# Kernel tuning notes

Measured on AMD Instinct MI355X. Metric: run time of the kernel, lower is better.

## Reference

```python
import jax, jax.numpy as jnp
import numpy as np

B, T, D, H, Z = 256, 256, 512, 1024, 128
EPS = 1e-6


def _init_params(key):
    ks = jax.random.split(key, 30)
    def w(i, fi, fo):
        return 0.02 * jax.random.normal(ks[i], (fi, fo), dtype=jnp.float32)
    def b(i, fo):
        return 0.01 * jax.random.normal(ks[i], (fo,), dtype=jnp.float32)
    return {
        'phix_w': w(0, D, H), 'phix_b': b(1, H),
        'pm_w1': w(2, H, H), 'pm_b1': b(3, H), 'pm_w2': w(4, H, Z), 'pm_b2': b(5, Z),
        'ps_w1': w(6, H, H), 'ps_b1': b(7, H), 'ps_w2': w(8, H, Z), 'ps_b2': b(9, Z),
        'em_w1': w(10, 2 * H, H), 'em_b1': b(11, H), 'em_w2': w(12, H, Z), 'em_b2': b(13, Z),
        'es_w1': w(14, 2 * H, H), 'es_b1': b(15, H), 'es_w2': w(16, H, Z), 'es_b2': b(17, Z),
        'dm_w1': w(18, H + Z, H), 'dm_b1': b(19, H), 'dm_w2': w(20, H, D), 'dm_b2': b(21, D),
        'gru_wih': w(22, H + Z, 3 * H), 'gru_bih': b(23, 3 * H), 'gru_bhh': b(24, 3 * H),
    }


def setup_inputs() -> dict:
    key = jax.random.key(0)
    kx, ke, kh, kp = jax.random.split(key, 4)
    inp = {
        'x': jax.random.uniform(kx, (B, T, D), dtype=jnp.float32),   # bernoulli-like data in [0,1]
        'eps': jax.random.normal(ke, (T, B, Z), dtype=jnp.float32),  # reparam noise per step
        'h0': jax.random.normal(kh, (B, H), dtype=jnp.float32),      # Variable(th.randn) initial hidden
    }
    inp.update(_init_params(kp))
    return inp


def reference(x, eps, h0, phix_w, phix_b, pm_w1, pm_b1, pm_w2, pm_b2,
              ps_w1, ps_b1, ps_w2, ps_b2, em_w1, em_b1, em_w2, em_b2,
              es_w1, es_b1, es_w2, es_b2, dm_w1, dm_b1, dm_w2, dm_b2,
              gru_wih, gru_bih, gru_bhh):
    relu, sig, sp = jax.nn.relu, jax.nn.sigmoid, jax.nn.softplus

    def step(h, inp):
        x_t, e_t = inp                                            # [B,D], [B,Z]
        phi = relu(x_t @ phix_w + phix_b)                         # phi_x(x_t): [B,H]
        pm = relu(relu(h @ pm_w1 + pm_b1) @ pm_w2 + pm_b2)        # prior mu [B,Z]
        ps = sp(relu(h @ ps_w1 + ps_b1) @ ps_w2 + ps_b2)          # prior std [B,Z]
        hx = jnp.concatenate([h, phi], axis=-1)                   # [B,2H]
        zm = relu(relu(hx @ em_w1 + em_b1) @ em_w2 + em_b2)       # encoder mu
        zs = sp(relu(hx @ es_w1 + es_b1) @ es_w2 + es_b2)         # encoder std
        z = zm + zs * e_t                                         # reparam sample
        hz = jnp.concatenate([h, z], axis=-1)                     # [B,H+Z]
        xm = sig(relu(hz @ dm_w1 + dm_b1) @ dm_w2 + dm_b2)        # decoder mu [B,D]
        # GRU step; source calls self.rnn(...) without a hidden state -> h_prev = 0,
        # so the W_hh@h term vanishes and only b_hh contributes.
        gi = jnp.concatenate([phi, z], axis=-1) @ gru_wih + gru_bih
        gi_r, gi_u, gi_n = jnp.split(gi, 3, axis=-1)
        bh_r, bh_u, bh_n = jnp.split(gru_bhh, 3)
        r = sig(gi_r + bh_r)
        u = sig(gi_u + bh_u)
        n = jnp.tanh(gi_n + r * bh_n)
        h_new = (1.0 - u) * n                                     # (1-u)*n + u*0
        # ELBO: KL(q||p) for diagonal Gaussians + Bernoulli NLL, mean over batch
        kld = jnp.sum(jnp.log(ps + EPS) - jnp.log(zs + EPS)
                      + (zs ** 2 + (zm - pm) ** 2) / (2.0 * ps ** 2 + EPS) - 0.5,
                      axis=-1).mean()
        xm_c = jnp.clip(xm, 1e-6, 1.0 - 1e-6)
        nll = -jnp.sum(x_t * jnp.log(xm_c) + (1.0 - x_t) * jnp.log1p(-xm_c), axis=-1).mean()
        return h_new, (z, zm, zs, xm, kld + nll, kld, nll)

    xs = jnp.swapaxes(x, 0, 1)                                    # [T,B,D]
    _, (Zs, enc_mu, enc_std, dec_mu, loss_t, kld_t, nll_t) = jax.lax.scan(step, h0, (xs, eps))
    loss = loss_t.sum()
    return loss, kld_t[-1], nll_t[-1], Zs, enc_mu, enc_std, dec_mu
```

## Files before the change

kernel.cpp:

```cpp
#include <hip/hip_runtime.h>

typedef unsigned short u16;
typedef __bf16 bf16x8 __attribute__((ext_vector_type(8)));
typedef float f32x4 __attribute__((ext_vector_type(4)));
typedef unsigned uint32x4 __attribute__((ext_vector_type(4)));

#define EPSC 1e-6f

__device__ __forceinline__ float b2f(u16 x) { return __uint_as_float(((unsigned)x) << 16); }
__device__ __forceinline__ u16 f2b(float f) {
    unsigned u = __float_as_uint(f);
    unsigned r = (u + 0x7fffu + ((u >> 16) & 1u)) >> 16;
    return (u16)r;
}
__device__ __forceinline__ float softplusf(float x) {
    return fmaxf(x, 0.f) + log1pf(__expf(-fabsf(x)));
}

__global__ void conv_x4(u16* __restrict__ dst, const float* __restrict__ x) {
    size_t i4 = (size_t)blockIdx.x * 256 + threadIdx.x;
    size_t o = i4 * 4;
    int d = (int)(o & 511);
    int b = (int)((o >> 9) & 255);
    int t = (int)(o >> 17);
    float4 v = *(const float4*)(x + ((size_t)b * 256 + t) * 512 + d);
    unsigned p0 = (unsigned)f2b(v.x) | ((unsigned)f2b(v.y) << 16);
    unsigned p1 = (unsigned)f2b(v.z) | ((unsigned)f2b(v.w) << 16);
    *(uint2*)(dst + o) = make_uint2(p0, p1);
}

__global__ void conv_f32_bf16(u16* __restrict__ dst, const float* __restrict__ src, int n) {
    int i = blockIdx.x * 256 + threadIdx.x;
    if (i < n) dst[i] = f2b(src[i]);
}

__global__ void tr_conv(u16* __restrict__ dst, const float* __restrict__ src,
                        int R, int C, int ld) {
    int idx = blockIdx.x * 256 + threadIdx.x;
    if (idx >= R * C) return;
    int c = idx / R, r = idx % R;
    dst[idx] = f2b(src[(size_t)r * ld + c]);
}

__global__ void conv_fragB(u16* __restrict__ dst, const float* __restrict__ em1,
                           const float* __restrict__ es1) {
    int idx = blockIdx.x * 256 + threadIdx.x;
    int col = idx >> 8, kb = idx & 255;
    int k = kb * 8, ct = col >> 4, lr = col & 15, kq = kb >> 2, lk = kb & 3;
    size_t off = ((size_t)ct * 64 + kq) * 512 + lk * 128 + lr * 8;
    const float* src = (col < 1024) ? em1 : es1;
    const int c = (col < 1024) ? col : col - 1024;
#pragma unroll
    for (int j = 0; j < 8; j++)
        dst[off + j] = f2b(src[(size_t)(k + j) * 1024 + c]);
}

__global__ void conv_fragB2(u16* __restrict__ dst, const float* __restrict__ src) {
    int idx = blockIdx.x * 256 + threadIdx.x;
    int col = idx >> 7, kb = idx & 127;
    int k = kb * 8, ct = col >> 4, lr = col & 15, kq = kb >> 2, lk = kb & 3;
    size_t off = ((size_t)ct * 32 + kq) * 512 + lk * 128 + lr * 8;
#pragma unroll
    for (int j = 0; j < 8; j++)
        dst[off + j] = f2b(src[(size_t)(k + j) * 128 + col]);
}

__global__ void conv_fragG(u16* __restrict__ dst, const float* __restrict__ gwih) {
    int idx = blockIdx.x * 256 + threadIdx.x;
    int gate = idx >> 14, rem = idx & 16383;
    int col = rem >> 4, kb = rem & 15;
    int k = kb * 8, ct = col >> 4, lr = col & 15, kq = kb >> 2, lk = kb & 3;
    size_t off = (size_t)gate * 131072 + ((size_t)ct * 4 + kq) * 512 + lk * 128 + lr * 8;
#pragma unroll
    for (int j = 0; j < 8; j++)
        dst[off + j] = f2b(gwih[(size_t)(1024 + k + j) * 3072 + gate * 1024 + col]);
}

enum { EPI_PARTIAL = 0, EPI_BF16_RELU = 1, EPI_BF16_NONE = 2,
       EPI_F32_RELU = 3, EPI_F32_SP = 4, EPI_F32_SIG = 5, EPI_TGIP = 6 };

template <int EPI>
__global__ __launch_bounds__(256)
void gemm128(const u16* __restrict__ A0, const u16* __restrict__ A1,
             int lda0, int lda1, int kSplit,
             const u16* __restrict__ Wt, int ldw,
             const float* __restrict__ bias,
             u16* __restrict__ Cb, float* __restrict__ Cf,
             int M, int N, int K, int kChunk) {
    __shared__ __align__(16) u16 As[128 * 72];
    __shared__ __align__(16) u16 Bs[128 * 72];
    const int tid = threadIdx.x;
    const int wid = tid >> 6, lane = tid & 63;
    const int wm = wid >> 1, wn = wid & 1;
    const int lr = lane & 15, lk = lane >> 4;
    const int m0 = blockIdx.y * 128, n0 = blockIdx.x * 128;
    const int kBeg = blockIdx.z * kChunk;
    const int rsub = lane >> 3;
    const int csub = (lane & 7) * 8;

    f32x4 acc[4][4];
#pragma unroll
    for (int i = 0; i < 4; i++)
#pragma unroll
        for (int j = 0; j < 4; j++) { f32x4 z = {0.f, 0.f, 0.f, 0.f}; acc[i][j] = z; }

    for (int kt = 0; kt < kChunk; kt += 64) {
        const int k0 = kBeg + kt;
        const u16* Ap; int kk, lda;
        if (k0 < kSplit) { Ap = A0; kk = k0; lda = lda0; }
        else             { Ap = A1; kk = k0 - kSplit; lda = lda1; }
        uint4 ra[4], rb[4];
#pragma unroll
        for (int i = 0; i < 4; i++) {
            const int q = wid * 4 + i;
            const int r = q * 8 + rsub;
            ra[i] = *(const uint4*)(Ap + (size_t)(m0 + r) * lda + kk + csub);
            rb[i] = *(const uint4*)(Wt + (size_t)(n0 + r) * ldw + k0 + csub);
        }
        __syncthreads();
#pragma unroll
        for (int i = 0; i < 4; i++) {
            const int q = wid * 4 + i;
            const int r = q * 8 + rsub;
            *(uint4*)&As[r * 72 + csub] = ra[i];
            *(uint4*)&Bs[r * 72 + csub] = rb[i];
        }
        __syncthreads();
#pragma unroll
        for (int s = 0; s < 2; s++) {
            bf16x8 af[4], bfr[4];
#pragma unroll
            for (int i = 0; i < 4; i++)
                af[i] = *(const bf16x8*)&As[(wm * 64 + i * 16 + lr) * 72 + s * 32 + lk * 8];
#pragma unroll
            for (int j = 0; j < 4; j++)
                bfr[j] = *(const bf16x8*)&Bs[(wn * 64 + j * 16 + lr) * 72 + s * 32 + lk * 8];
#pragma unroll
            for (int i = 0; i < 4; i++)
#pragma unroll
                for (int j = 0; j < 4; j++)
                    acc[i][j] = __builtin_amdgcn_mfma_f32_16x16x32_bf16(af[i], bfr[j], acc[i][j], 0, 0, 0);
        }
    }

    const int rowb = m0 + wm * 64, colb = n0 + wn * 64;
#pragma unroll
    for (int i = 0; i < 4; i++) {
#pragma unroll
        for (int j = 0; j < 4; j++) {
            const int col = colb + j * 16 + lr;
            if (EPI == EPI_TGIP) {
                const int row0 = rowb + i * 16 + lk * 4;
                const int tt = row0 >> 8, b0 = row0 & 255;
                const int gate = col >> 10, cc = col & 1023;
                unsigned lo = (unsigned)f2b(acc[i][j][0]) | ((unsigned)f2b(acc[i][j][1]) << 16);
                unsigned hi = (unsigned)f2b(acc[i][j][2]) | ((unsigned)f2b(acc[i][j][3]) << 16);
                *(uint2*)(Cb + (((size_t)tt * 3 + gate) * 1024 + cc) * 256 + b0) = make_uint2(lo, hi);
            } else {
#pragma unroll
                for (int r = 0; r < 4; r++) {
                    const int row = rowb + i * 16 + lk * 4 + r;
                    float v = acc[i][j][r];
                    if (EPI == EPI_PARTIAL) {
                        Cf[(size_t)blockIdx.z * ((size_t)M * N) + (size_t)row * N + col] = v;
                    } else {
                        if (bias) v += bias[col];
                        if (EPI == EPI_BF16_RELU || EPI == EPI_F32_RELU) v = fmaxf(v, 0.f);
                        else if (EPI == EPI_F32_SP)  v = softplusf(v);
                        else if (EPI == EPI_F32_SIG) v = 1.f / (1.f + __expf(-v));
                        if (EPI == EPI_BF16_RELU || EPI == EPI_BF16_NONE) Cb[(size_t)row * N + col] = f2b(v);
                        else Cf[(size_t)row * N + col] = v;
                    }
                }
            }
        }
    }
}

static constexpr size_t oPHIXWT  = 0;
static constexpr size_t oWCATT   = 1048576;
static constexpr size_t oEMW2T   = 9437184;
static constexpr size_t oESW2T   = 9699328;
static constexpr size_t oWIHPHIT = 9961472;
static constexpr size_t oWIHZT   = 16252928;
static constexpr size_t oPMW1T   = 17039360;
static constexpr size_t oPMW2T   = 19136512;
static constexpr size_t oPSW1T   = 19398656;
static constexpr size_t oPSW2T   = 21495808;
static constexpr size_t oDMW1T   = 21757952;
static constexpr size_t oDMW2T   = 24117248;
static constexpr size_t oHS      = 25165824;
static constexpr size_t oZBF     = 159907840;
static constexpr size_t oT12     = 176685056;
static constexpr size_t oBAR     = 177733632;
static constexpr size_t oKLDT    = 177737728;
static constexpr size_t oNLLT    = 177738752;
static constexpr size_t oPHI     = 177739776;
static constexpr size_t oGIP     = 311957504;
static constexpr size_t WS_NEED  = 714610688;

static constexpr size_t NZ = (size_t)256 * 256 * 128;
static constexpr size_t O_Z  = 3;
static constexpr size_t O_MU = 3 + NZ;
static constexpr size_t O_STD = 3 + 2 * NZ;
static constexpr size_t O_XM = 3 + 3 * NZ;

__global__ __launch_bounds__(256, 1)
void vrnn_step(int t, int prolog,
               const float* __restrict__ eps,
               const float* __restrict__ em_b1, const float* __restrict__ es_b1,
               const float* __restrict__ em_b2, const float* __restrict__ es_b2,
               const float* __restrict__ gbih, const float* __restrict__ gbhh,
               char* ws, float* out) {
    __shared__ __align__(16) u16 POOL[16 * 2056];
    __shared__ float zmL[2048], zsL[2048];
    __shared__ __align__(16) u16 zTH[16 * 136];

    const int bx = blockIdx.x, tid = threadIdx.x;
    const int wid = tid >> 6, lane = tid & 63;
    const int lr = lane & 15, lk = lane >> 4;
    const int g = bx >> 4, n = bx & 15;
    const int r0 = g * 16;

    const u16* wcatF = (const u16*)(ws + oWCATT);
    const u16* em2F  = (const u16*)(ws + oEMW2T);
    const u16* es2F  = (const u16*)(ws + oESW2T);
    const u16* wihZF = (const u16*)(ws + oWIHZT);
    const u16* PHI   = (const u16*)(ws + oPHI);
    const u16* GIPT  = (const u16*)(ws + oGIP);
    u16* HS    = (u16*)(ws + oHS);
    u16* ZBFg  = (u16*)(ws + oZBF);
    u16* T12p0 = (u16*)(ws + oT12);
    u16* T12p1 = (u16*)(ws + oPHIXWT);

    float* outZ  = out + O_Z;
    float* outMu = out + O_MU;
    float* outSd = out + O_STD;

    u16* S12 = POOL;
    u16* hL  = POOL;
    u16* PH  = POOL + 16 * 1032;

    const int srow = tid >> 4, sc8 = (tid & 15) * 8;

    if (!prolog) {
        {
            const u16* src = ((t & 1) ? T12p1 : T12p0) + (size_t)(r0 + srow) * 2048 + sc8;
#pragma unroll
            for (int p = 0; p < 16; p++)
                *(uint32x4*)&S12[srow * 2056 + sc8 + p * 128] = *(const uint32x4*)(src + p * 128);
        }
        __syncthreads();

        {
            const int halfz = wid >> 1, cq = wid & 1;
            const u16* WF = (halfz ? es2F : em2F) + (size_t)(cq * 4) * 16384 + lk * 128 + lr * 8;
            const u16* Sr = &S12[lr * 2056 + halfz * 1024];
            f32x4 az0 = {0.f,0.f,0.f,0.f}, az1 = az0, az2 = az0, az3 = az0;
#pragma unroll 1
            for (int kq = 0; kq < 32; kq++) {
                bf16x8 af = *(const bf16x8*)(Sr + kq * 32 + lk * 8);
                az0 = __builtin_amdgcn_mfma_f32_16x16x32_bf16(af, *(const bf16x8*)(WF + (size_t)kq * 512), az0, 0, 0, 0);
                az1 = __builtin_amdgcn_mfma_f32_16x16x32_bf16(af, *(const bf16x8*)(WF + 16384 + (size_t)kq * 512), az1, 0, 0, 0);
                az2 = __builtin_amdgcn_mfma_f32_16x16x32_bf16(af, *(const bf16x8*)(WF + 32768 + (size_t)kq * 512), az2, 0, 0, 0);
                az3 = __builtin_amdgcn_mfma_f32_16x16x32_bf16(af, *(const bf16x8*)(WF + 49152 + (size_t)kq * 512), az3, 0, 0, 0);
            }
#pragma unroll
            for (int q = 0; q < 4; q++) {
                const f32x4 az = (q == 0) ? az0 : (q == 1) ? az1 : (q == 2) ? az2 : az3;
                const int c = cq * 64 + q * 16 + lr;
#pragma unroll
                for (int r = 0; r < 4; r++) {
                    const int row = lk * 4 + r;
                    if (!halfz) zmL[row * 128 + c] = fmaxf(az[r] + em_b2[c], 0.f);
                    else        zsL[row * 128 + c] = softplusf(az[r] + es_b2[c]);
                }
            }
        }
        __syncthreads();

        {
            const int row = tid >> 4, col = (tid & 15) * 8;
            const size_t o = (size_t)t * 32768 + (size_t)(r0 + row) * 128 + col;
            const float* ep = eps + o;
            float4 e0 = *(const float4*)ep, e1 = *(const float4*)(ep + 4);
            float zmv[8], zsv[8], zv[8];
#pragma unroll
            for (int i = 0; i < 8; i++) {
                zmv[i] = zmL[row * 128 + col + i];
                zsv[i] = zsL[row * 128 + col + i];
                const float ev = (i < 4) ? (&e0.x)[i] : (&e1.x)[i - 4];
                zv[i] = zmv[i] + zsv[i] * ev;
            }
            uint32x4 zp;
#pragma unroll
            for (int j = 0; j < 4; j++)
                zp[j] = (unsigned)f2b(zv[2 * j]) | ((unsigned)f2b(zv[2 * j + 1]) << 16);
            *(uint32x4*)&zTH[row * 136 + col] = zp;
            if (n == 0) {
#pragma unroll
                for (int i = 0; i < 8; i++) {
                    outMu[o + i] = zmv[i];
                    outSd[o + i] = zsv[i];
                    outZ[o + i]  = zv[i];
                }
                *(uint32x4*)(ZBFg + o) = zp;
            }
        }
        __syncthreads();

        {
            bf16x8 zf0 = *(const bf16x8*)&zTH[lr * 136 + lk * 8];
            bf16x8 zf1 = *(const bf16x8*)&zTH[lr * 136 + 32 + lk * 8];
            bf16x8 zf2 = *(const bf16x8*)&zTH[lr * 136 + 64 + lk * 8];
            bf16x8 zf3 = *(const bf16x8*)&zTH[lr * 136 + 96 + lk * 8];
            const u16* gT = GIPT + (size_t)t * 786432;
#pragma unroll 1
            for (int i = 0; i < 16; i++) {
                const int ct = wid * 16 + i;
                const int col = ct * 16 + lr;
                const u16* bR = wihZF + (size_t)ct * 2048 + lk * 128 + lr * 8;
                const u16* bU = bR + 131072;
                const u16* bN = bU + 131072;
                f32x4 aR = {0.f,0.f,0.f,0.f}, aU = aR, aN = aR;
                aR = __builtin_amdgcn_mfma_f32_16x16x32_bf16(zf0, *(const bf16x8*)(bR), aR, 0, 0, 0);
                aR = __builtin_amdgcn_mfma_f32_16x16x32_bf16(zf1, *(const bf16x8*)(bR + 512), aR, 0, 0, 0);
                aR = __builtin_amdgcn_mfma_f32_16x16x32_bf16(zf2, *(const bf16x8*)(bR + 1024), aR, 0, 0, 0);
                aR = __builtin_amdgcn_mfma_f32_16x16x32_bf16(zf3, *(const bf16x8*)(bR + 1536), aR, 0, 0, 0);
                aU = __builtin_amdgcn_mfma_f32_16x16x32_bf16(zf0, *(const bf16x8*)(bU), aU, 0, 0, 0);
                aU = __builtin_amdgcn_mfma_f32_16x16x32_bf16(zf1, *(const bf16x8*)(bU + 512), aU, 0, 0, 0);
                aU = __builtin_amdgcn_mfma_f32_16x16x32_bf16(zf2, *(const bf16x8*)(bU + 1024), aU, 0, 0, 0);
                aU = __builtin_amdgcn_mfma_f32_16x16x32_bf16(zf3, *(const bf16x8*)(bU + 1536), aU, 0, 0, 0);
                aN = __builtin_amdgcn_mfma_f32_16x16x32_bf16(zf0, *(const bf16x8*)(bN), aN, 0, 0, 0);
                aN = __builtin_amdgcn_mfma_f32_16x16x32_bf16(zf1, *(const bf16x8*)(bN + 512), aN, 0, 0, 0);
                aN = __builtin_amdgcn_mfma_f32_16x16x32_bf16(zf2, *(const bf16x8*)(bN + 1024), aN, 0, 0, 0);
                aN = __builtin_amdgcn_mfma_f32_16x16x32_bf16(zf3, *(const bf16x8*)(bN + 1536), aN, 0, 0, 0);
                const size_t gb = (size_t)col * 256 + r0 + lk * 4;
                uint2 gR2 = *(const uint2*)(gT + gb);
                uint2 gU2 = *(const uint2*)(gT + 262144 + gb);
                uint2 gN2 = *(const uint2*)(gT + 524288 + gb);
                const u16 gRv[4] = {(u16)(gR2.x & 0xffff), (u16)(gR2.x >> 16),
                                    (u16)(gR2.y & 0xffff), (u16)(gR2.y >> 16)};
                const u16 gUv[4] = {(u16)(gU2.x & 0xffff), (u16)(gU2.x >> 16),
                                    (u16)(gU2.y & 0xffff), (u16)(gU2.y >> 16)};
                const u16 gNv[4] = {(u16)(gN2.x & 0xffff), (u16)(gN2.x >> 16),
                                    (u16)(gN2.y & 0xffff), (u16)(gN2.y >> 16)};
                const float bihR = gbih[col],        bhR = gbhh[col];
                const float bihU = gbih[1024 + col], bhU = gbhh[1024 + col];
                const float bihN = gbih[2048 + col], bhN = gbhh[2048 + col];
#pragma unroll
                for (int r = 0; r < 4; r++) {
                    const float gr = aR[r] + b2f(gRv[r]) + bihR + bhR;
                    const float gu = aU[r] + b2f(gUv[r]) + bihU + bhU;
                    float gn       = aN[r] + b2f(gNv[r]) + bihN;
                    const float rr_ = 1.f / (1.f + __expf(-gr));
                    const float uu  = 1.f / (1.f + __expf(-gu));
                    gn += rr_ * bhN;
                    const float e2 = __expf(-2.f * fabsf(gn));
                    float th = (1.f - e2) / (1.f + e2);
                    th = (gn < 0.f) ? -th : th;
                    hL[(lk * 4 + r) * 1032 + col] = f2b((1.f - uu) * th);
                }
            }
        }
        __syncthreads();

        if (n == 0) {
            u16* dstH = HS + (size_t)(t + 1) * 262144 + (size_t)(r0 + srow) * 1024 + sc8;
#pragma unroll
            for (int p = 0; p < 8; p++)
                *(uint32x4*)(dstH + p * 128) = *(const uint32x4*)&hL[srow * 1032 + sc8 + p * 128];
        }
    } else {
        const u16* src = HS + (size_t)(r0 + srow) * 1024 + sc8;
#pragma unroll
        for (int p = 0; p < 8; p++)
            *(uint32x4*)&hL[srow * 1032 + sc8 + p * 128] = *(const uint32x4*)(src + p * 128);
        __syncthreads();
    }

    if (t < 255) {
        {
            const u16* psrc = PHI + (size_t)(t + 1) * 262144 + (size_t)(r0 + srow) * 1024 + sc8;
#pragma unroll
            for (int p = 0; p < 8; p++)
                *(uint32x4*)&PH[srow * 1032 + sc8 + p * 128] = *(const uint32x4*)(psrc + p * 128);
        }
        __syncthreads();

        f32x4 a0 = {0.f,0.f,0.f,0.f}, a1 = {0.f,0.f,0.f,0.f};
        const int ct0 = n * 8 + wid * 2;
        const u16* b0s = wcatF + (size_t)ct0 * 32768 + lk * 128 + lr * 8;
        const u16* b1s = b0s + 32768;
#pragma unroll 1
        for (int kq = 0; kq < 32; kq++) {
            bf16x8 af = *(const bf16x8*)&hL[lr * 1032 + kq * 32 + lk * 8];
            a0 = __builtin_amdgcn_mfma_f32_16x16x32_bf16(af, *(const bf16x8*)(b0s + (size_t)kq * 512), a0, 0, 0, 0);
            a1 = __builtin_amdgcn_mfma_f32_16x16x32_bf16(af, *(const bf16x8*)(b1s + (size_t)kq * 512), a1, 0, 0, 0);
        }
#pragma unroll 1
        for (int kq = 32; kq < 64; kq++) {
            bf16x8 af = *(const bf16x8*)&PH[lr * 1032 + (kq - 32) * 32 + lk * 8];
            a0 = __builtin_amdgcn_mfma_f32_16x16x32_bf16(af, *(const bf16x8*)(b0s + (size_t)kq * 512), a0, 0, 0, 0);
            a1 = __builtin_amdgcn_mfma_f32_16x16x32_bf16(af, *(const bf16x8*)(b1s + (size_t)kq * 512), a1, 0, 0, 0);
        }
        __syncthreads();
#pragma unroll
        for (int i = 0; i < 2; i++) {
            const f32x4 a = i ? a1 : a0;
            const int lct = wid * 2 + i;
            const int colg = n * 128 + lct * 16 + lr;
            const float bb = (colg < 1024) ? em_b1[colg] : es_b1[colg - 1024];
#pragma unroll
            for (int r = 0; r < 4; r++)
                zTH[(lk * 4 + r) * 136 + lct * 16 + lr] = f2b(fmaxf(a[r] + bb, 0.f));
        }
        __syncthreads();
        {
            u16* dst = ((t & 1) ? T12p0 : T12p1) + (size_t)(r0 + srow) * 2048 + n * 128 + sc8;
            *(uint32x4*)dst = *(const uint32x4*)&zTH[srow * 136 + sc8];
        }
    }
}

__global__ __launch_bounds__(256)
void loss_per_t(const float* __restrict__ x,
                const float* __restrict__ xm,
                const float* __restrict__ zm, const float* __restrict__ zs,
                const float* __restrict__ pm, const float* __restrict__ ps,
                float* __restrict__ kldT, float* __restrict__ nllT) {
    const int t = blockIdx.x, bb = threadIdx.x;
    float kld = 0.f, nll = 0.f;
    const size_t ozb = ((size_t)t * 256 + bb) * 128;
    for (int zz = 0; zz < 128; zz++) {
        const float qs = zs[ozb + zz], qm = zm[ozb + zz];
        const float pmv = pm[ozb + zz], psv = ps[ozb + zz];
        const float d = qm - pmv;
        kld += logf(psv + EPSC) - logf(qs + EPSC)
             + (qs * qs + d * d) / (2.f * psv * psv + EPSC) - 0.5f;
    }
    const size_t oxb = ((size_t)t * 256 + bb) * 512;
    const size_t oxi = ((size_t)bb * 256 + t) * 512;
    for (int dd = 0; dd < 512; dd++) {
        const float xv = x[oxi + dd];
        float m = xm[oxb + dd];
        m = fminf(fmaxf(m, 1e-6f), 1.f - 1e-6f);
        nll -= xv * logf(m) + (1.f - xv) * log1pf(-m);
    }
    __shared__ float sk[256], sn[256];
    sk[bb] = kld; sn[bb] = nll;
    __syncthreads();
    for (int s = 128; s > 0; s >>= 1) {
        if (bb < s) { sk[bb] += sk[bb + s]; sn[bb] += sn[bb + s]; }
        __syncthreads();
    }
    if (bb == 0) { kldT[t] = sk[0] / 256.f; nllT[t] = sn[0] / 256.f; }
}

__global__ __launch_bounds__(256)
void loss_final(const float* __restrict__ kldT, const float* __restrict__ nllT,
                float* __restrict__ out) {
    const int tid = threadIdx.x;
    __shared__ float s[256];
    s[tid] = kldT[tid] + nllT[tid];
    __syncthreads();
    for (int st = 128; st > 0; st >>= 1) {
        if (tid < st) s[tid] += s[tid + st];
        __syncthreads();
    }
    if (tid == 0) { out[0] = s[0]; out[1] = kldT[255]; out[2] = nllT[255]; }
}

extern "C" void kernel_launch(void* const* d_in, const int* in_sizes, int n_in,
                              void* d_out, int out_size, void* d_ws, size_t ws_size,
                              hipStream_t stream) {
    const float* x      = (const float*)d_in[0];
    const float* eps    = (const float*)d_in[1];
    const float* h0     = (const float*)d_in[2];
    const float* phix_w = (const float*)d_in[3];
    const float* phix_b = (const float*)d_in[4];
    const float* pm_w1  = (const float*)d_in[5];
    const float* pm_b1  = (const float*)d_in[6];
    const float* pm_w2  = (const float*)d_in[7];
    const float* pm_b2  = (const float*)d_in[8];
    const float* ps_w1  = (const float*)d_in[9];
    const float* ps_b1  = (const float*)d_in[10];
    const float* ps_w2  = (const float*)d_in[11];
    const float* ps_b2  = (const float*)d_in[12];
    const float* em_w1  = (const float*)d_in[13];
    const float* em_b1  = (const float*)d_in[14];
    const float* em_w2  = (const float*)d_in[15];
    const float* em_b2  = (const float*)d_in[16];
    const float* es_w1  = (const float*)d_in[17];
    const float* es_b1  = (const float*)d_in[18];
    const float* es_w2  = (const float*)d_in[19];
    const float* es_b2  = (const float*)d_in[20];
    const float* dm_w1  = (const float*)d_in[21];
    const float* dm_b1  = (const float*)d_in[22];
    const float* dm_w2  = (const float*)d_in[23];
    const float* dm_b2  = (const float*)d_in[24];
    const float* gwih   = (const float*)d_in[25];
    const float* gbih   = (const float*)d_in[26];
    const float* gbhh   = (const float*)d_in[27];
    float* out = (float*)d_out;

    if (ws_size < WS_NEED) return;
    char* w = (char*)d_ws;
    u16* phixWt  = (u16*)(w + oPHIXWT);
    u16* wcatF   = (u16*)(w + oWCATT);
    u16* em2F    = (u16*)(w + oEMW2T);
    u16* es2F    = (u16*)(w + oESW2T);
    u16* wihPhiT = (u16*)(w + oWIHPHIT);
    u16* wihZF   = (u16*)(w + oWIHZT);
    u16* pmW1T   = (u16*)(w + oPMW1T);
    u16* pmW2T   = (u16*)(w + oPMW2T);
    u16* psW1T   = (u16*)(w + oPSW1T);
    u16* psW2T   = (u16*)(w + oPSW2T);
    u16* dmW1T   = (u16*)(w + oDMW1T);
    u16* dmW2T   = (u16*)(w + oDMW2T);
    u16* HS      = (u16*)(w + oHS);
    u16* ZBF     = (u16*)(w + oZBF);
    u16* PHI     = (u16*)(w + oPHI);
    u16* GIPT    = (u16*)(w + oGIP);
    u16* XbfT    = (u16*)(w + oGIP);
    float* PMbuf = (float*)(w + oGIP);
    float* PSbuf = (float*)(w + oGIP + 33554432);
    float* kldT  = (float*)(w + oKLDT);
    float* nllT  = (float*)(w + oNLLT);

    conv_x4<<<32768, 256, 0, stream>>>(XbfT, x);
    conv_f32_bf16<<<1024, 256, 0, stream>>>(HS, h0, 262144);
    tr_conv<<<2048, 256, 0, stream>>>(phixWt, phix_w, 512, 1024, 1024);
    conv_fragB<<<2048, 256, 0, stream>>>(wcatF, em_w1, es_w1);
    conv_fragB2<<<64, 256, 0, stream>>>(em2F, em_w2);
    conv_fragB2<<<64, 256, 0, stream>>>(es2F, es_w2);
    tr_conv<<<12288, 256, 0, stream>>>(wihPhiT, gwih, 1024, 3072, 3072);
    conv_fragG<<<192, 256, 0, stream>>>(wihZF, gwih);
    tr_conv<<<4096, 256, 0, stream>>>(pmW1T, pm_w1, 1024, 1024, 1024);
    tr_conv<<<512, 256, 0, stream>>>(pmW2T, pm_w2, 1024, 128, 128);
    tr_conv<<<4096, 256, 0, stream>>>(psW1T, ps_w1, 1024, 1024, 1024);
    tr_conv<<<512, 256, 0, stream>>>(psW2T, ps_w2, 1024, 128, 128);
    tr_conv<<<4608, 256, 0, stream>>>(dmW1T, dm_w1, 1152, 1024, 1024);
    tr_conv<<<2048, 256, 0, stream>>>(dmW2T, dm_w2, 1024, 512, 512);

    gemm128<EPI_BF16_RELU><<<dim3(8, 512, 1), 256, 0, stream>>>(
        XbfT, nullptr, 512, 0, 512, phixWt, 512, phix_b, PHI, nullptr, 65536, 1024, 512, 512);
    gemm128<EPI_TGIP><<<dim3(24, 512, 1), 256, 0, stream>>>(
        PHI, nullptr, 1024, 0, 1024, wihPhiT, 1024, nullptr, GIPT, nullptr, 65536, 3072, 1024, 1024);

    vrnn_step<<<256, 256, 0, stream>>>(-1, 1, eps, em_b1, es_b1, em_b2, es_b2,
                                       gbih, gbhh, (char*)d_ws, out);
    for (int t = 0; t < 256; t++)
        vrnn_step<<<256, 256, 0, stream>>>(t, 0, eps, em_b1, es_b1, em_b2, es_b2,
                                           gbih, gbhh, (char*)d_ws, out);

    gemm128<EPI_BF16_RELU><<<dim3(8, 512, 1), 256, 0, stream>>>(
        HS, nullptr, 1024, 0, 1024, pmW1T, 1024, pm_b1, PHI, nullptr, 65536, 1024, 1024, 1024);
    gemm128<EPI_F32_RELU><<<dim3(1, 512, 1), 256, 0, stream>>>(
        PHI, nullptr, 1024, 0, 1024, pmW2T, 1024, pm_b2, nullptr, PMbuf, 65536, 128, 1024, 1024);
    gemm128<EPI_BF16_RELU><<<dim3(8, 512, 1), 256, 0, stream>>>(
        HS, nullptr, 1024, 0, 1024, psW1T, 1024, ps_b1, PHI, nullptr, 65536, 1024, 1024, 1024);
    gemm128<EPI_F32_SP><<<dim3(1, 512, 1), 256, 0, stream>>>(
        PHI, nullptr, 1024, 0, 1024, psW2T, 1024, ps_b2, nullptr, PSbuf, 65536, 128, 1024, 1024);
    gemm128<EPI_BF16_RELU><<<dim3(8, 512, 1), 256, 0, stream>>>(
        HS, ZBF, 1024, 128, 1024, dmW1T, 1152, dm_b1, PHI, nullptr, 65536, 1024, 1152, 1152);
    gemm128<EPI_F32_SIG><<<dim3(4, 512, 1), 256, 0, stream>>>(
        PHI, nullptr, 1024, 0, 1024, dmW2T, 1024, dm_b2, nullptr, out + O_XM, 65536, 512, 1024, 1024);

    loss_per_t<<<256, 256, 0, stream>>>(x, out + O_XM, out + O_MU, out + O_STD,
                                        PMbuf, PSbuf, kldT, nllT);
    loss_final<<<1, 256, 0, stream>>>(kldT, nllT, out);
}
```

Before: 21.34 ms.

## Split recurrent step into two kernels and partition GRU columns across blocks

The fused per-step kernel is split into two launches per timestep. The first computes the encoder first layer across 256 blocks. The second runs the encoder second layer, reparameterization and GRU update on 64 blocks, with each group of four blocks splitting the GRU output columns. Before, every block redundantly recomputed the full second-layer and GRU work for its row group, so this cuts that duplication. It also remaps block indices in the first kernel. The cost is twice as many kernel launches per step, plus a global round trip for the hidden state and intermediate activations between launches.

New measurement: 17.58 ms. -17.6%, faster.

```diff
diff --git a/kernel.cpp b/kernel.cpp
--- a/kernel.cpp
+++ b/kernel.cpp
@@ -206,220 +206,236 @@
 static constexpr size_t O_XM = 3 + 3 * NZ;
 
 __global__ __launch_bounds__(256, 1)
-void vrnn_step(int t, int prolog,
-               const float* __restrict__ eps,
-               const float* __restrict__ em_b1, const float* __restrict__ es_b1,
-               const float* __restrict__ em_b2, const float* __restrict__ es_b2,
-               const float* __restrict__ gbih, const float* __restrict__ gbhh,
-               char* ws, float* out) {
-    __shared__ __align__(16) u16 POOL[16 * 2056];
-    __shared__ float zmL[2048], zsL[2048];
-    __shared__ __align__(16) u16 zTH[16 * 136];
+void vrnn_w1(int t, const float* __restrict__ em_b1, const float* __restrict__ es_b1,
+             char* ws) {
+    __shared__ __align__(16) u16 hL[16 * 1032];
+    __shared__ __align__(16) u16 PH[16 * 1032];
+    __shared__ __align__(16) u16 TH16[16 * 136];
 
     const int bx = blockIdx.x, tid = threadIdx.x;
     const int wid = tid >> 6, lane = tid & 63;
     const int lr = lane & 15, lk = lane >> 4;
-    const int g = bx >> 4, n = bx & 15;
+    const int n = 2 * (bx & 7) + (bx >> 7);
+    const int g = (bx >> 3) & 15;
     const int r0 = g * 16;
 
     const u16* wcatF = (const u16*)(ws + oWCATT);
+    const u16* PHI   = (const u16*)(ws + oPHI);
+    const u16* HS    = (const u16*)(ws + oHS);
+    u16* T12g = (u16*)(ws + oT12);
+
+    const int srow = tid >> 4, sc8 = (tid & 15) * 8;
+
+    {
+        const u16* hs = HS + (size_t)t * 262144 + (size_t)(r0 + srow) * 1024 + sc8;
+        const u16* ps = PHI + (size_t)t * 262144 + (size_t)(r0 + srow) * 1024 + sc8;
+#pragma unroll
+        for (int p = 0; p < 8; p++) {
+            *(uint32x4*)&hL[srow * 1032 + sc8 + p * 128] = *(const uint32x4*)(hs + p * 128);
+            *(uint32x4*)&PH[srow * 1032 + sc8 + p * 128] = *(const uint32x4*)(ps + p * 128);
+        }
+    }
+    __syncthreads();
+
+    f32x4 a0 = {0.f,0.f,0.f,0.f}, a1 = {0.f,0.f,0.f,0.f};
+    const int ct0 = n * 8 + wid * 2;
+    const u16* b0s = wcatF + (size_t)ct0 * 32768 + lk * 128 + lr * 8;
+    const u16* b1s = b0s + 32768;
+#pragma unroll 1
+    for (int kq = 0; kq < 32; kq++) {
+        bf16x8 af = *(const bf16x8*)&hL[lr * 1032 + kq * 32 + lk * 8];
+        a0 = __builtin_amdgcn_mfma_f32_16x16x32_bf16(af, *(const bf16x8*)(b0s + (size_t)kq * 512), a0, 0, 0, 0);
+        a1 = __builtin_amdgcn_mfma_f32_16x16x32_bf16(af, *(const bf16x8*)(b1s + (size_t)kq * 512), a1, 0, 0, 0);
+    }
+#pragma unroll 1
+    for (int kq = 32; kq < 64; kq++) {
+        bf16x8 af = *(const bf16x8*)&PH[lr * 1032 + (kq - 32) * 32 + lk * 8];
+        a0 = __builtin_amdgcn_mfma_f32_16x16x32_bf16(af, *(const bf16x8*)(b0s + (size_t)kq * 512), a0, 0, 0, 0);
+        a1 = __builtin_amdgcn_mfma_f32_16x16x32_bf16(af, *(const bf16x8*)(b1s + (size_t)kq * 512), a1, 0, 0, 0);
+    }
+    __syncthreads();
+#pragma unroll
+    for (int i = 0; i < 2; i++) {
+        const f32x4 a = i ? a1 : a0;
+        const int lct = wid * 2 + i;
+        const int colg = n * 128 + lct * 16 + lr;
+        const float bb = (colg < 1024) ? em_b1[colg] : es_b1[colg - 1024];
+#pragma unroll
+        for (int r = 0; r < 4; r++)
+            TH16[(lk * 4 + r) * 136 + lct * 16 + lr] = f2b(fmaxf(a[r] + bb, 0.f));
+    }
+    __syncthreads();
+    *(uint32x4*)(T12g + (size_t)(r0 + srow) * 2048 + n * 128 + sc8) =
+        *(const uint32x4*)&TH16[srow * 136 + sc8];
+}
+
+__global__ __launch_bounds__(256, 1)
+void vrnn_w23(int t,
+              const float* __restrict__ eps,
+              const float* __restrict__ em_b2, const float* __restrict__ es_b2,
+              const float* __restrict__ gbih, const float* __restrict__ gbhh,
+              char* ws, float* out) {
+    __shared__ __align__(16) u16 S12[16 * 2056];
+    __shared__ float zmL[2048], zsL[2048];
+    __shared__ __align__(16) u16 zTH[16 * 136];
+
+    const int bx = blockIdx.x, tid = threadIdx.x;
+    const int wid = tid >> 6, lane = tid & 63;
+    const int lr = lane & 15, lk = lane >> 4;
+    const int q = bx & 3, g = bx >> 2;
+    const int r0 = g * 16;
+
     const u16* em2F  = (const u16*)(ws + oEMW2T);
     const u16* es2F  = (const u16*)(ws + oESW2T);
     const u16* wihZF = (const u16*)(ws + oWIHZT);
-    const u16* PHI   = (const u16*)(ws + oPHI);
     const u16* GIPT  = (const u16*)(ws + oGIP);
-    u16* HS    = (u16*)(ws + oHS);
-    u16* ZBFg  = (u16*)(ws + oZBF);
-    u16* T12p0 = (u16*)(ws + oT12);
-    u16* T12p1 = (u16*)(ws + oPHIXWT);
+    u16* HS   = (u16*)(ws + oHS);
+    u16* ZBFg = (u16*)(ws + oZBF);
+    u16* T12g = (u16*)(ws + oT12);
 
     float* outZ  = out + O_Z;
     float* outMu = out + O_MU;
     float* outSd = out + O_STD;
 
-    u16* S12 = POOL;
-    u16* hL  = POOL;
-    u16* PH  = POOL + 16 * 1032;
+    u16* hT = S12;
 
     const int srow = tid >> 4, sc8 = (tid & 15) * 8;
 
-    if (!prolog) {
-        {
-            const u16* src = ((t & 1) ? T12p1 : T12p0) + (size_t)(r0 + srow) * 2048 + sc8;
-#pragma unroll
-            for (int p = 0; p < 16; p++)
-                *(uint32x4*)&S12[srow * 2056 + sc8 + p * 128] = *(const uint32x4*)(src + p * 128);
-        }
-        __syncthreads();
-
-        {
-            const int halfz = wid >> 1, cq = wid & 1;
-            const u16* WF = (halfz ? es2F : em2F) + (size_t)(cq * 4) * 16384 + lk * 128 + lr * 8;
-            const u16* Sr = &S12[lr * 2056 + halfz * 1024];
-            f32x4 az0 = {0.f,0.f,0.f,0.f}, az1 = az0, az2 = az0, az3 = az0;
-#pragma unroll 1
-            for (int kq = 0; kq < 32; kq++) {
-                bf16x8 af = *(const bf16x8*)(Sr + kq * 32 + lk * 8);
-                az0 = __builtin_amdgcn_mfma_f32_16x16x32_bf16(af, *(const bf16x8*)(WF + (size_t)kq * 512), az0, 0, 0, 0);
-                az1 = __builtin_amdgcn_mfma_f32_16x16x32_bf16(af, *(const bf16x8*)(WF + 16384 + (size_t)kq * 512), az1, 0, 0, 0);
-                az2 = __builtin_amdgcn_mfma_f32_16x16x32_bf16(af, *(const bf16x8*)(WF + 32768 + (size_t)kq * 512), az2, 0, 0, 0);
-                az3 = __builtin_amdgcn_mfma_f32_16x16x32_bf16(af, *(const bf16x8*)(WF + 49152 + (size_t)kq * 512), az3, 0, 0, 0);
-            }
-#pragma unroll
-            for (int q = 0; q < 4; q++) {
-                const f32x4 az = (q == 0) ? az0 : (q == 1) ? az1 : (q == 2) ? az2 : az3;
-                const int c = cq * 64 + q * 16 + lr;
-#pragma unroll
-                for (int r = 0; r < 4; r++) {
-                    const int row = lk * 4 + r;
-                    if (!halfz) zmL[row * 128 + c] = fmaxf(az[r] + em_b2[c], 0.f);
-                    else        zsL[row * 128 + c] = softplusf(az[r] + es_b2[c]);
-                }
-            }
-        }
-        __syncthreads();
-
-        {
-            const int row = tid >> 4, col = (tid & 15) * 8;
-            const size_t o = (size_t)t * 32768 + (size_t)(r0 + row) * 128 + col;
-            const float* ep = eps + o;
-            float4 e0 = *(const float4*)ep, e1 = *(const float4*)(ep + 4);
-            float zmv[8], zsv[8], zv[8];
-#pragma unroll
-            for (int i = 0; i < 8; i++) {
-                zmv[i] = zmL[row * 128 + col + i];
-                zsv[i] = zsL[row * 128 + col + i];
-                const float ev = (i < 4) ? (&e0.x)[i] : (&e1.x)[i - 4];
-                zv[i] = zmv[i] + zsv[i] * ev;
-            }
-            uint32x4 zp;
-#pragma unroll
-            for (int j = 0; j < 4; j++)
-                zp[j] = (unsigned)f2b(zv[2 * j]) | ((unsigned)f2b(zv[2 * j + 1]) << 16);
-            *(uint32x4*)&zTH[row * 136 + col] = zp;
-            if (n == 0) {
-#pragma unroll
-                for (int i = 0; i < 8; i++) {
-                    outMu[o + i] = zmv[i];
-                    outSd[o + i] = zsv[i];
-                    outZ[o + i]  = zv[i];
-                }
-                *(uint32x4*)(ZBFg + o) = zp;
-            }
-        }
-        __syncthreads();
-
-        {
-            bf16x8 zf0 = *(const bf16x8*)&zTH[lr * 136 + lk * 8];
-            bf16x8 zf1 = *(const bf16x8*)&zTH[lr * 136 + 32 + lk * 8];
-            bf16x8 zf2 = *(const bf16x8*)&zTH[lr * 136 + 64 + lk * 8];
-            bf16x8 zf3 = *(const bf16x8*)&zTH[lr * 136 + 96 + lk * 8];
-            const u16* gT = GIPT + (size_t)t * 786432;
-#pragma unroll 1
-            for (int i = 0; i < 16; i++) {
-                const int ct = wid * 16 + i;
-                const int col = ct * 16 + lr;
-                const u16* bR = wihZF + (size_t)ct * 2048 + lk * 128 + lr * 8;
-                const u16* bU = bR + 131072;
-                const u16* bN = bU + 131072;
-                f32x4 aR = {0.f,0.f,0.f,0.f}, aU = aR, aN = aR;
-                aR = __builtin_amdgcn_mfma_f32_16x16x32_bf16(zf0, *(const bf16x8*)(bR), aR, 0, 0, 0);
-                aR = __builtin_amdgcn_mfma_f32_16x16x32_bf16(zf1, *(const bf16x8*)(bR + 512), aR, 0, 0, 0);
-                aR = __builtin_amdgcn_mfma_f32_16x16x32_bf16(zf2, *(const bf16x8*)(bR + 1024), aR, 0, 0, 0);
-                aR = __builtin_amdgcn_mfma_f32_16x16x32_bf16(zf3, *(const bf16x8*)(bR + 1536), aR, 0, 0, 0);
-                aU = __builtin_amdgcn_mfma_f32_16x16x32_bf16(zf0, *(const bf16x8*)(bU), aU, 0, 0, 0);
-                aU = __builtin_amdgcn_mfma_f32_16x16x32_bf16(zf1, *(const bf16x8*)(bU + 512), aU, 0, 0, 0);
-                aU = __builtin_amdgcn_mfma_f32_16x16x32_bf16(zf2, *(const bf16x8*)(bU + 1024), aU, 0, 0, 0);
-                aU = __builtin_amdgcn_mfma_f32_16x16x32_bf16(zf3, *(const bf16x8*)(bU + 1536), aU, 0, 0, 0);
-                aN = __builtin_amdgcn_mfma_f32_16x16x32_bf16(zf0, *(const bf16x8*)(bN), aN, 0, 0, 0);
-                aN = __builtin_amdgcn_mfma_f32_16x16x32_bf16(zf1, *(const bf16x8*)(bN + 512), aN, 0, 0, 0);
-                aN = __builtin_amdgcn_mfma_f32_16x16x32_bf16(zf2, *(const bf16x8*)(bN + 1024), aN, 0, 0, 0);
-                aN = __builtin_amdgcn_mfma_f32_16x16x32_bf16(zf3, *(const bf16x8*)(bN + 1536), aN, 0, 0, 0);
-                const size_t gb = (size_t)col * 256 + r0 + lk * 4;
-                uint2 gR2 = *(const uint2*)(gT + gb);
-                uint2 gU2 = *(const uint2*)(gT + 262144 + gb);
-                uint2 gN2 = *(const uint2*)(gT + 524288 + gb);
-                const u16 gRv[4] = {(u16)(gR2.x & 0xffff), (u16)(gR2.x >> 16),
-                                    (u16)(gR2.y & 0xffff), (u16)(gR2.y >> 16)};
-                const u16 gUv[4] = {(u16)(gU2.x & 0xffff), (u16)(gU2.x >> 16),
-                                    (u16)(gU2.y & 0xffff), (u16)(gU2.y >> 16)};
-                const u16 gNv[4] = {(u16)(gN2.x & 0xffff), (u16)(gN2.x >> 16),
-                                    (u16)(gN2.y & 0xffff), (u16)(gN2.y >> 16)};
-                const float bihR = gbih[col],        bhR = gbhh[col];
-                const float bihU = gbih[1024 + col], bhU = gbhh[1024 + col];
-                const float bihN = gbih[2048 + col], bhN = gbhh[2048 + col];
-#pragma unroll
-                for (int r = 0; r < 4; r++) {
-                    const float gr = aR[r] + b2f(gRv[r]) + bihR + bhR;
-                    const float gu = aU[r] + b2f(gUv[r]) + bihU + bhU;
-                    float gn       = aN[r] + b2f(gNv[r]) + bihN;
-                    const float rr_ = 1.f / (1.f + __expf(-gr));
-                    const float uu  = 1.f / (1.f + __expf(-gu));
-                    gn += rr_ * bhN;
-                    const float e2 = __expf(-2.f * fabsf(gn));
-                    float th = (1.f - e2) / (1.f + e2);
-                    th = (gn < 0.f) ? -th : th;
-                    hL[(lk * 4 + r) * 1032 + col] = f2b((1.f - uu) * th);
-                }
-            }
-        }
-        __syncthreads();
-
-        if (n == 0) {
-            u16* dstH = HS + (size_t)(t + 1) * 262144 + (size_t)(r0 + srow) * 1024 + sc8;
-#pragma unroll
-            for (int p = 0; p < 8; p++)
-                *(uint32x4*)(dstH + p * 128) = *(const uint32x4*)&hL[srow * 1032 + sc8 + p * 128];
-        }
-    } else {
-        const u16* src = HS + (size_t)(r0 + srow) * 1024 + sc8;
-#pragma unroll
-        for (int p = 0; p < 8; p++)
-            *(uint32x4*)&hL[srow * 1032 + sc8 + p * 128] = *(const uint32x4*)(src + p * 128);
-        __syncthreads();
-    }
-
-    if (t < 255) {
-        {
-            const u16* psrc = PHI + (size_t)(t + 1) * 262144 + (size_t)(r0 + srow) * 1024 + sc8;
-#pragma unroll
-            for (int p = 0; p < 8; p++)
-                *(uint32x4*)&PH[srow * 1032 + sc8 + p * 128] = *(const uint32x4*)(psrc + p * 128);
-        }
-        __syncthreads();
-
-        f32x4 a0 = {0.f,0.f,0.f,0.f}, a1 = {0.f,0.f,0.f,0.f};
-        const int ct0 = n * 8 + wid * 2;
-        const u16* b0s = wcatF + (size_t)ct0 * 32768 + lk * 128 + lr * 8;
-        const u16* b1s = b0s + 32768;
+    {
+        const u16* src = T12g + (size_t)(r0 + srow) * 2048 + sc8;
+#pragma unroll
+        for (int p = 0; p < 16; p++)
+            *(uint32x4*)&S12[srow * 2056 + sc8 + p * 128] = *(const uint32x4*)(src + p * 128);
+    }
+    __syncthreads();
+
+    {
+        const int halfz = wid >> 1, cq = wid & 1;
+        const u16* WF = (halfz ? es2F : em2F) + (size_t)(cq * 4) * 16384 + lk * 128 + lr * 8;
+        const u16* Sr = &S12[lr * 2056 + halfz * 1024];
+        f32x4 az0 = {0.f,0.f,0.f,0.f}, az1 = az0, az2 = az0, az3 = az0;
 #pragma unroll 1
         for (int kq = 0; kq < 32; kq++) {
-            bf16x8 af = *(const bf16x8*)&hL[lr * 1032 + kq * 32 + lk * 8];
-            a0 = __builtin_amdgcn_mfma_f32_16x16x32_bf16(af, *(const bf16x8*)(b0s + (size_t)kq * 512), a0, 0, 0, 0);
-            a1 = __builtin_amdgcn_mfma_f32_16x16x32_bf16(af, *(const bf16x8*)(b1s + (size_t)kq * 512), a1, 0, 0, 0);
-        }
+            bf16x8 af = *(const bf16x8*)(Sr + kq * 32 + lk * 8);
+            az0 = __builtin_amdgcn_mfma_f32_16x16x32_bf16(af, *(const bf16x8*)(WF + (size_t)kq * 512), az0, 0, 0, 0);
+            az1 = __builtin_amdgcn_mfma_f32_16x16x32_bf16(af, *(const bf16x8*)(WF + 16384 + (size_t)kq * 512), az1, 0, 0, 0);
+            az2 = __builtin_amdgcn_mfma_f32_16x16x32_bf16(af, *(const bf16x8*)(WF + 32768 + (size_t)kq * 512), az2, 0, 0, 0);
+            az3 = __builtin_amdgcn_mfma_f32_16x16x32_bf16(af, *(const bf16x8*)(WF + 49152 + (size_t)kq * 512), az3, 0, 0, 0);
+        }
+#pragma unroll
+        for (int p = 0; p < 4; p++) {
+            const f32x4 az = (p == 0) ? az0 : (p == 1) ? az1 : (p == 2) ? az2 : az3;
+            const int c = cq * 64 + p * 16 + lr;
+#pragma unroll
+            for (int r = 0; r < 4; r++) {
+                const int row = lk * 4 + r;
+                if (!halfz) zmL[row * 128 + c] = fmaxf(az[r] + em_b2[c], 0.f);
+                else        zsL[row * 128 + c] = softplusf(az[r] + es_b2[c]);
+            }
+        }
+    }
+    __syncthreads();
+
+    {
+        const int row = tid >> 4, col = (tid & 15) * 8;
+        const size_t o = (size_t)t * 32768 + (size_t)(r0 + row) * 128 + col;
+        const float* ep = eps + o;
+        float4 e0 = *(const float4*)ep, e1 = *(const float4*)(ep + 4);
+        float zmv[8], zsv[8], zv[8];
+#pragma unroll
+        for (int i = 0; i < 8; i++) {
+            zmv[i] = zmL[row * 128 + col + i];
+            zsv[i] = zsL[row * 128 + col + i];
+            const float ev = (i < 4) ? (&e0.x)[i] : (&e1.x)[i - 4];
+            zv[i] = zmv[i] + zsv[i] * ev;
+        }
+        uint32x4 zp;
+#pragma unroll
+        for (int j = 0; j < 4; j++)
+            zp[j] = (unsigned)f2b(zv[2 * j]) | ((unsigned)f2b(zv[2 * j + 1]) << 16);
+        *(uint32x4*)&zTH[row * 136 + col] = zp;
+        if (q == 0) {
+#pragma unroll
+            for (int i = 0; i < 8; i++) {
+                outMu[o + i] = zmv[i];
+                outSd[o + i] = zsv[i];
+                outZ[o + i]  = zv[i];
+            }
+            *(uint32x4*)(ZBFg + o) = zp;
+        }
+    }
+    __syncthreads();
+
+    {
+        bf16x8 zf0 = *(const bf16x8*)&zTH[lr * 136 + lk * 8];
+        bf16x8 zf1 = *(const bf16x8*)&zTH[lr * 136 + 32 + lk * 8];
+        bf16x8 zf2 = *(const bf16x8*)&zTH[lr * 136 + 64 + lk * 8];
+        bf16x8 zf3 = *(const bf16x8*)&zTH[lr * 136 + 96 + lk * 8];
+        const u16* gT = GIPT + (size_t)t * 786432;
+        u16 hout[4][4];
 #pragma unroll 1
-        for (int kq = 32; kq < 64; kq++) {
-            bf16x8 af = *(const bf16x8*)&PH[lr * 1032 + (kq - 32) * 32 + lk * 8];
-            a0 = __builtin_amdgcn_mfma_f32_16x16x32_bf16(af, *(const bf16x8*)(b0s + (size_t)kq * 512), a0, 0, 0, 0);
-            a1 = __builtin_amdgcn_mfma_f32_16x16x32_bf16(af, *(const bf16x8*)(b1s + (size_t)kq * 512), a1, 0, 0, 0);
+        for (int i = 0; i < 4; i++) {
+            const int ct = q * 16 + wid * 4 + i;
+            const int col = ct * 16 + lr;
+            const u16* bR = wihZF + (size_t)ct * 2048 + lk * 128 + lr * 8;
+            const u16* bU = bR + 131072;
+            const u16* bN = bU + 131072;
+            f32x4 aR = {0.f,0.f,0.f,0.f}, aU = aR, aN = aR;
+            aR = __builtin_amdgcn_mfma_f32_16x16x32_bf16(zf0, *(const bf16x8*)(bR), aR, 0, 0, 0);
+            aR = __builtin_amdgcn_mfma_f32_16x16x32_bf16(zf1, *(const bf16x8*)(bR + 512), aR, 0, 0, 0);
+            aR = __builtin_amdgcn_mfma_f32_16x16x32_bf16(zf2, *(const bf16x8*)(bR + 1024), aR, 0, 0, 0);
+            aR = __builtin_amdgcn_mfma_f32_16x16x32_bf16(zf3, *(const bf16x8*)(bR + 1536), aR, 0, 0, 0);
+            aU = __builtin_amdgcn_mfma_f32_16x16x32_bf16(zf0, *(const bf16x8*)(bU), aU, 0, 0, 0);
+            aU = __builtin_amdgcn_mfma_f32_16x16x32_bf16(zf1, *(const bf16x8*)(bU + 512), aU, 0, 0, 0);
+            aU = __builtin_amdgcn_mfma_f32_16x16x32_bf16(zf2, *(const bf16x8*)(bU + 1024), aU, 0, 0, 0);
+            aU = __builtin_amdgcn_mfma_f32_16x16x32_bf16(zf3, *(const bf16x8*)(bU + 1536), aU, 0, 0, 0);
+            aN = __builtin_amdgcn_mfma_f32_16x16x32_bf16(zf0, *(const bf16x8*)(bN), aN, 0, 0, 0);
+            aN = __builtin_amdgcn_mfma_f32_16x16x32_bf16(zf1, *(const bf16x8*)(bN + 512), aN, 0, 0, 0);
+            aN = __builtin_amdgcn_mfma_f32_16x16x32_bf16(zf2, *(const bf16x8*)(bN + 1024), aN, 0, 0, 0);
+            aN = __builtin_amdgcn_mfma_f32_16x16x32_bf16(zf3, *(const bf16x8*)(bN + 1536), aN, 0, 0, 0);
+            const size_t gb = (size_t)col * 256 + r0 + lk * 4;
+            uint2 gR2 = *(const uint2*)(gT + gb);
+            uint2 gU2 = *(const uint2*)(gT + 262144 + gb);
+            uint2 gN2 = *(const uint2*)(gT + 524288 + gb);
+            const u16 gRv[4] = {(u16)(gR2.x & 0xffff), (u16)(gR2.x >> 16),
+                                (u16)(gR2.y & 0xffff), (u16)(gR2.y >> 16)};
+            const u16 gUv[4] = {(u16)(gU2.x & 0xffff), (u16)(gU2.x >> 16),
+                                (u16)(gU2.y & 0xffff), (u16)(gU2.y >> 16)};
+            const u16 gNv[4] = {(u16)(gN2.x & 0xffff), (u16)(gN2.x >> 16),
+                                (u16)(gN2.y & 0xffff), (u16)(gN2.y >> 16)};
+            const float bihR = gbih[col],        bhR = gbhh[col];
+            const float bihU = gbih[1024 + col], bhU = gbhh[1024 + col];
+            const float bihN = gbih[2048 + col], bhN = gbhh[2048 + col];
+#pragma unroll
+            for (int r = 0; r < 4; r++) {
+                const float gr = aR[r] + b2f(gRv[r]) + bihR + bhR;
+                const float gu = aU[r] + b2f(gUv[r]) + bihU + bhU;
+                float gn       = aN[r] + b2f(gNv[r]) + bihN;
+                const float rr_ = 1.f / (1.f + __expf(-gr));
+                const float uu  = 1.f / (1.f + __expf(-gu));
+                gn += rr_ * bhN;
+                const float e2 = __expf(-2.f * fabsf(gn));
+                float th = (1.f - e2) / (1.f + e2);
+                th = (gn < 0.f) ? -th : th;
+                hout[i][r] = f2b((1.f - uu) * th);
+            }
         }
         __syncthreads();
 #pragma unroll
-        for (int i = 0; i < 2; i++) {
-            const f32x4 a = i ? a1 : a0;
-            const int lct = wid * 2 + i;
-            const int colg = n * 128 + lct * 16 + lr;
-            const float bb = (colg < 1024) ? em_b1[colg] : es_b1[colg - 1024];
+        for (int i = 0; i < 4; i++) {
+            const int lct = wid * 4 + i;
 #pragma unroll
             for (int r = 0; r < 4; r++)
-                zTH[(lk * 4 + r) * 136 + lct * 16 + lr] = f2b(fmaxf(a[r] + bb, 0.f));
-        }
-        __syncthreads();
-        {
-            u16* dst = ((t & 1) ? T12p0 : T12p1) + (size_t)(r0 + srow) * 2048 + n * 128 + sc8;
-            *(uint32x4*)dst = *(const uint32x4*)&zTH[srow * 136 + sc8];
-        }
+                hT[(lk * 4 + r) * 264 + lct * 16 + lr] = hout[i][r];
+        }
+    }
+    __syncthreads();
+
+    {
+        const int row = tid >> 4, c16 = (tid & 15) * 16;
+        u16* dst = HS + (size_t)(t + 1) * 262144 + (size_t)(r0 + row) * 1024 + q * 256 + c16;
+        *(uint32x4*)dst       = *(const uint32x4*)&hT[row * 264 + c16];
+        *(uint32x4*)(dst + 8) = *(const uint32x4*)&hT[row * 264 + c16 + 8];
     }
 }
 
@@ -548,11 +564,11 @@
     gemm128<EPI_TGIP><<<dim3(24, 512, 1), 256, 0, stream>>>(
         PHI, nullptr, 1024, 0, 1024, wihPhiT, 1024, nullptr, GIPT, nullptr, 65536, 3072, 1024, 1024);
 
-    vrnn_step<<<256, 256, 0, stream>>>(-1, 1, eps, em_b1, es_b1, em_b2, es_b2,
-                                       gbih, gbhh, (char*)d_ws, out);
-    for (int t = 0; t < 256; t++)
-        vrnn_step<<<256, 256, 0, stream>>>(t, 0, eps, em_b1, es_b1, em_b2, es_b2,
-                                           gbih, gbhh, (char*)d_ws, out);
+    for (int t = 0; t < 256; t++) {
+        vrnn_w1<<<256, 256, 0, stream>>>(t, em_b1, es_b1, (char*)d_ws);
+        vrnn_w23<<<64, 256, 0, stream>>>(t, eps, em_b2, es_b2, gbih, gbhh,
+                                         (char*)d_ws, out);
+    }
 
     gemm128<EPI_BF16_RELU><<<dim3(8, 512, 1), 256, 0, stream>>>(
         HS, nullptr, 1024, 0, 1024, pmW1T, 1024, pm_b1, PHI, nullptr, 65536, 1024, 1024, 1024);
```
